# Performance work log

Measured on AMD Instinct MI355X. Metric: run time of the kernel, lower is better.

The kernel has to match this reference:

```python
import jax, jax.numpy as jnp
import numpy as np

B, S, D = 4, 1024, 1024      # batch, seq_len, hidden_size
I = 4096                     # intermediate_size
E = 8                        # num_experts
K = 2                        # top-k


def setup_inputs() -> dict:
    key = jax.random.key(0)
    ks = jax.random.split(key, 8)
    x = jax.random.normal(ks[0], (B, S, D), dtype=jnp.float32)
    gate_w = jax.random.normal(ks[1], (E, D), dtype=jnp.float32) * 0.02
    gate_b = jnp.zeros((E,), dtype=jnp.float32)
    w1 = jax.random.normal(ks[2], (E, I, D), dtype=jnp.float32) * 0.02
    b1 = jnp.zeros((E, I), dtype=jnp.float32)
    w2 = jax.random.normal(ks[3], (E, D, I), dtype=jnp.float32) * 0.02
    b2 = jnp.zeros((E, D), dtype=jnp.float32)
    return {"x": x, "gate_w": gate_w, "gate_b": gate_b,
            "w1": w1, "b1": b1, "w2": w2, "b2": b2}


def reference(x, gate_w, gate_b, w1, b1, w2, b2):
    b, s, d = x.shape
    xf = x.reshape(-1, d)                                  # [N, D]
    logits = xf @ gate_w.T + gate_b                        # [N, E]
    top_vals, top_idx = jax.lax.top_k(logits, K)           # [N, K]
    top_w = jax.nn.softmax(top_vals, axis=-1)              # softmax over the k selected logits

    # combine[n, e] = routing weight of token n for expert e (0 if not selected)
    n_tok = xf.shape[0]
    combine = jnp.zeros((n_tok, w1.shape[0]), dtype=x.dtype)
    combine = combine.at[jnp.arange(n_tok)[:, None], top_idx].add(top_w)

    out = jnp.zeros_like(xf)
    for e in range(w1.shape[0]):                           # small fixed loop over experts
        h = jax.nn.gelu(xf @ w1[e].T + b1[e], approximate=False)  # exact GELU (torch default)
        out = out + combine[:, e:e + 1] * (h @ w2[e].T + b2[e])
    return out.reshape(b, s, d)
```

## Files before the change

kernel.cpp:

```cpp
#include <hip/hip_runtime.h>
#include <math.h>

#define NTOK 4096
#define DDIM 1024
#define IDIM 4096
#define NEXP 8
#define MAXPAD 9216

typedef _Float16 f16x8 __attribute__((ext_vector_type(8)));
typedef _Float16 f16x4 __attribute__((ext_vector_type(4)));
typedef float    f32x4 __attribute__((ext_vector_type(4)));

__device__ __forceinline__ void glds16(const _Float16* g, _Float16* l) {
    __builtin_amdgcn_global_load_lds(
        (const __attribute__((address_space(1))) _Float16*)g,
        (__attribute__((address_space(3))) _Float16*)l, 16, 0, 0);
}

__device__ __forceinline__ float fast_gelu(float v) {
    float u = v * (0.7978845608f + 0.0356774081f * v * v);
    float ex = __builtin_amdgcn_exp2f(u * 2.8853900817779268f);
    float th = 1.0f - 2.0f * __builtin_amdgcn_rcpf(ex + 1.0f);
    return 0.5f * v * (1.0f + th);
}

__global__ void cvt_kernel(const float* __restrict__ src, _Float16* __restrict__ dst, int n4) {
    int i = blockIdx.x * blockDim.x + threadIdx.x;
    if (i >= n4) return;
    float4 v = ((const float4*)src)[i];
    f16x4 o = { (_Float16)v.x, (_Float16)v.y, (_Float16)v.z, (_Float16)v.w };
    ((f16x4*)dst)[i] = o;
}

__global__ void gate_kernel(const float* __restrict__ x, const float* __restrict__ gw,
                            const float* __restrict__ gb,
                            int* __restrict__ cnt, int* __restrict__ tok,
                            float* __restrict__ wgt) {
    int wave = threadIdx.x >> 6;
    int lane = threadIdx.x & 63;
    int token = blockIdx.x * 4 + wave;
    const float* xr = x + (size_t)token * DDIM;
    float xv[16];
#pragma unroll
    for (int j = 0; j < 16; ++j) xv[j] = xr[lane + 64 * j];
    float lg[NEXP];
#pragma unroll
    for (int e = 0; e < NEXP; ++e) {
        const float* g = gw + e * DDIM;
        float s = 0.f;
#pragma unroll
        for (int j = 0; j < 16; ++j) s += xv[j] * g[lane + 64 * j];
#pragma unroll
        for (int o = 32; o > 0; o >>= 1) s += __shfl_xor(s, o, 64);
        lg[e] = s + gb[e];
    }
    if (lane == 0) {
        int i0 = 0; float v0 = lg[0];
        for (int e = 1; e < NEXP; ++e) if (lg[e] > v0) { v0 = lg[e]; i0 = e; }
        int i1 = -1; float v1 = -3.0e38f;
        for (int e = 0; e < NEXP; ++e) { if (e == i0) continue; if (lg[e] > v1) { v1 = lg[e]; i1 = e; } }
        float e1 = expf(v1 - v0);
        float den = 1.f + e1;
        float w0 = 1.f / den;
        float w1 = e1 / den;
        int p0 = atomicAdd(&cnt[i0], 1);
        tok[i0 * NTOK + p0] = token; wgt[i0 * NTOK + p0] = w0;
        int p1 = atomicAdd(&cnt[i1], 1);
        tok[i1 * NTOK + p1] = token; wgt[i1 * NTOK + p1] = w1;
    }
}

__global__ void scan_kernel(const int* __restrict__ cnt, int* __restrict__ off) {
    if (threadIdx.x == 0) {
        int acc = 0;
        for (int e = 0; e < NEXP; ++e) { off[e] = acc; acc += ((cnt[e] + 127) >> 7) << 7; }
        off[NEXP] = acc;
    }
}

__global__ void gather_kernel(const float* __restrict__ x, const int* __restrict__ cnt,
                              const int* __restrict__ off, const int* __restrict__ tok,
                              _Float16* __restrict__ xg) {
    int row = blockIdx.x;
    if (row >= off[NEXP]) return;
    int e = 0;
    while (e < NEXP - 1 && row >= off[e + 1]) ++e;
    int r = row - off[e];
    int t = threadIdx.x;
    _Float16* dst = xg + (size_t)row * DDIM;
    if (r < cnt[e]) {
        int token = tok[e * NTOK + r];
        float4 v = ((const float4*)(x + (size_t)token * DDIM))[t];
        f16x4 o = { (_Float16)v.x, (_Float16)v.y, (_Float16)v.z, (_Float16)v.w };
        ((f16x4*)dst)[t] = o;
    } else {
        f16x4 z = {};
        ((f16x4*)dst)[t] = z;
    }
}

template <int KDIM, int NDIM, int NT, int EPI, int SPLIT>
__global__ __launch_bounds__(256, 4) void gemm_kernel(
    const _Float16* __restrict__ A,
    const _Float16* __restrict__ Bw,
    const float* __restrict__ bias,
    const int* __restrict__ cnt, const int* __restrict__ off,
    const int* __restrict__ tok, const float* __restrict__ wgt,
    _Float16* __restrict__ Hout, float* __restrict__ Out) {
    int e  = blockIdx.z / SPLIT;
    int kc = blockIdx.z % SPLIT;
    const int KB = KDIM / SPLIT;
    int nt = blockIdx.x % NT;
    int mt = blockIdx.x / NT;
    int ce = cnt[e];
    int mtiles = (ce + 127) >> 7;
    if (mt >= mtiles) return;
    int rowbase = off[e] + mt * 128;
    int colbase = nt * 128;

    __shared__ __align__(16) _Float16 As[128 * 32];
    __shared__ __align__(16) _Float16 Bs[128 * 32];

    int tid = threadIdx.x;
    int wv = tid >> 6, lane = tid & 63;
    int wm = (wv >> 1) * 64, wn = (wv & 1) * 64;

    const _Float16* Abase = A + (size_t)rowbase * KDIM + kc * KB;
    const _Float16* Bbase = Bw + (size_t)e * NDIM * KDIM + (size_t)colbase * KDIM + kc * KB;

    int ldrow = wv * 32 + (lane >> 2);
    int ldcol = (lane & 3) * 8;

    int fr = lane & 15;
    int fk = (lane >> 4) * 8;

    f32x4 acc[4][4] = {};

    for (int k0 = 0; k0 < KB; k0 += 32) {
        __syncthreads();
        glds16(Abase + (size_t)ldrow * KDIM + k0 + ldcol,        &As[(wv * 32) * 32]);
        glds16(Abase + (size_t)(ldrow + 16) * KDIM + k0 + ldcol, &As[(wv * 32 + 16) * 32]);
        glds16(Bbase + (size_t)ldrow * KDIM + k0 + ldcol,        &Bs[(wv * 32) * 32]);
        glds16(Bbase + (size_t)(ldrow + 16) * KDIM + k0 + ldcol, &Bs[(wv * 32 + 16) * 32]);
        __syncthreads();
        f16x8 a[4], b[4];
#pragma unroll
        for (int i = 0; i < 4; ++i) a[i] = *(const f16x8*)&As[(wm + i * 16 + fr) * 32 + fk];
#pragma unroll
        for (int j = 0; j < 4; ++j) b[j] = *(const f16x8*)&Bs[(wn + j * 16 + fr) * 32 + fk];
#pragma unroll
        for (int i = 0; i < 4; ++i)
#pragma unroll
            for (int j = 0; j < 4; ++j)
                acc[i][j] = __builtin_amdgcn_mfma_f32_16x16x32_f16(a[i], b[j], acc[i][j], 0, 0, 0);
    }

    int rquad = (lane >> 4) * 4;
    if (EPI == 1) {
#pragma unroll
        for (int i = 0; i < 4; ++i) {
#pragma unroll
            for (int j = 0; j < 4; ++j) {
                int col = colbase + wn + j * 16 + fr;
                float bb = bias[e * NDIM + col];
#pragma unroll
                for (int r = 0; r < 4; ++r) {
                    int ml = wm + i * 16 + rquad + r;
                    float v = fast_gelu(acc[i][j][r] + bb);
                    Hout[(size_t)(rowbase + ml) * NDIM + col] = (_Float16)v;
                }
            }
        }
    } else {
#pragma unroll
        for (int i = 0; i < 4; ++i) {
#pragma unroll
            for (int r = 0; r < 4; ++r) {
                int ml = wm + i * 16 + rquad + r;
                int slot = mt * 128 + ml;
                if (slot < ce) {
                    int token = tok[e * NTOK + slot];
                    float w = wgt[e * NTOK + slot];
#pragma unroll
                    for (int j = 0; j < 4; ++j) {
                        int col = colbase + wn + j * 16 + fr;
                        float v = acc[i][j][r];
                        if (kc == 0) v += bias[e * NDIM + col];
                        unsafeAtomicAdd(&Out[(size_t)token * NDIM + col], w * v);
                    }
                }
            }
        }
    }
}

extern "C" void kernel_launch(void* const* d_in, const int* in_sizes, int n_in,
                              void* d_out, int out_size, void* d_ws, size_t ws_size,
                              hipStream_t stream) {
    const float* x      = (const float*)d_in[0];
    const float* gate_w = (const float*)d_in[1];
    const float* gate_b = (const float*)d_in[2];
    const float* w1     = (const float*)d_in[3];
    const float* b1     = (const float*)d_in[4];
    const float* w2     = (const float*)d_in[5];
    const float* b2     = (const float*)d_in[6];
    float* out = (float*)d_out;

    char* p = (char*)d_ws;
    _Float16* w1h  = (_Float16*)p; p += (size_t)NEXP * IDIM * DDIM * 2;
    _Float16* w2h  = (_Float16*)p; p += (size_t)NEXP * DDIM * IDIM * 2;
    _Float16* xg   = (_Float16*)p; p += (size_t)MAXPAD * DDIM * 2;
    _Float16* hbuf = (_Float16*)p; p += (size_t)MAXPAD * IDIM * 2;
    int*      tok  = (int*)p;      p += (size_t)NEXP * NTOK * 4;
    float*    wgt  = (float*)p;    p += (size_t)NEXP * NTOK * 4;
    int*      cnt  = (int*)p;      p += 128;
    int*      off  = (int*)p;      p += 128;

    hipMemsetAsync(cnt, 0, 128, stream);
    hipMemsetAsync(out, 0, (size_t)NTOK * DDIM * 4, stream);

    cvt_kernel<<<32768, 256, 0, stream>>>(w1, w1h, NEXP * IDIM * DDIM / 4);
    cvt_kernel<<<32768, 256, 0, stream>>>(w2, w2h, NEXP * DDIM * IDIM / 4);
    gate_kernel<<<NTOK / 4, 256, 0, stream>>>(x, gate_w, gate_b, cnt, tok, wgt);
    scan_kernel<<<1, 64, 0, stream>>>(cnt, off);
    gather_kernel<<<MAXPAD, 256, 0, stream>>>(x, cnt, off, tok, xg);

    gemm_kernel<DDIM, IDIM, IDIM / 128, 1, 1><<<dim3(32 * (IDIM / 128), 1, NEXP), 256, 0, stream>>>(
        xg, w1h, b1, cnt, off, tok, wgt, hbuf, (float*)nullptr);
    gemm_kernel<IDIM, DDIM, DDIM / 128, 2, 4><<<dim3(32 * (DDIM / 128), 1, NEXP * 4), 256, 0, stream>>>(
        hbuf, w2h, b2, cnt, off, tok, wgt, (_Float16*)nullptr, out);
}
```

Before: 701.0 us.

## Use persistent GEMM blocks with atomic tile counter over real expert tiles

Precomputes per-expert tile offsets in the scan kernel and turns both expert GEMMs into persistent kernels with 1024 blocks that fetch work tiles from a global atomic counter. This removes the many empty blocks launched for worst-case padding and balances the uneven per-expert work. It adds an atomic and two barriers per tile, and tiles are taken in a fixed order that may reduce cache locality.

New measurement: 744.0 us. +6.1%, slower.

```diff
diff --git a/kernel.cpp b/kernel.cpp
--- a/kernel.cpp
+++ b/kernel.cpp
@@ -72,9 +72,14 @@
 
 __global__ void scan_kernel(const int* __restrict__ cnt, int* __restrict__ off) {
     if (threadIdx.x == 0) {
-        int acc = 0;
-        for (int e = 0; e < NEXP; ++e) { off[e] = acc; acc += ((cnt[e] + 127) >> 7) << 7; }
-        off[NEXP] = acc;
+        int acc = 0, t1 = 0, t2 = 0;
+        for (int e = 0; e < NEXP; ++e) {
+            int mtiles = (cnt[e] + 127) >> 7;
+            off[e] = acc;       acc += mtiles << 7;
+            off[10 + e] = t1;   t1 += mtiles * (IDIM / 128);
+            off[20 + e] = t2;   t2 += mtiles * (DDIM / 128) * 4;
+        }
+        off[NEXP] = acc; off[10 + NEXP] = t1; off[20 + NEXP] = t2;
     }
 }
 
@@ -106,87 +111,98 @@
     const float* __restrict__ bias,
     const int* __restrict__ cnt, const int* __restrict__ off,
     const int* __restrict__ tok, const float* __restrict__ wgt,
-    _Float16* __restrict__ Hout, float* __restrict__ Out) {
-    int e  = blockIdx.z / SPLIT;
-    int kc = blockIdx.z % SPLIT;
+    _Float16* __restrict__ Hout, float* __restrict__ Out,
+    int* __restrict__ counter, const int* __restrict__ toff) {
     const int KB = KDIM / SPLIT;
-    int nt = blockIdx.x % NT;
-    int mt = blockIdx.x / NT;
-    int ce = cnt[e];
-    int mtiles = (ce + 127) >> 7;
-    if (mt >= mtiles) return;
-    int rowbase = off[e] + mt * 128;
-    int colbase = nt * 128;
 
     __shared__ __align__(16) _Float16 As[128 * 32];
     __shared__ __align__(16) _Float16 Bs[128 * 32];
+    __shared__ int s_tile;
 
     int tid = threadIdx.x;
     int wv = tid >> 6, lane = tid & 63;
     int wm = (wv >> 1) * 64, wn = (wv & 1) * 64;
-
-    const _Float16* Abase = A + (size_t)rowbase * KDIM + kc * KB;
-    const _Float16* Bbase = Bw + (size_t)e * NDIM * KDIM + (size_t)colbase * KDIM + kc * KB;
-
     int ldrow = wv * 32 + (lane >> 2);
     int ldcol = (lane & 3) * 8;
-
     int fr = lane & 15;
     int fk = (lane >> 4) * 8;
-
-    f32x4 acc[4][4] = {};
-
-    for (int k0 = 0; k0 < KB; k0 += 32) {
+    int total = toff[NEXP];
+
+    while (true) {
         __syncthreads();
-        glds16(Abase + (size_t)ldrow * KDIM + k0 + ldcol,        &As[(wv * 32) * 32]);
-        glds16(Abase + (size_t)(ldrow + 16) * KDIM + k0 + ldcol, &As[(wv * 32 + 16) * 32]);
-        glds16(Bbase + (size_t)ldrow * KDIM + k0 + ldcol,        &Bs[(wv * 32) * 32]);
-        glds16(Bbase + (size_t)(ldrow + 16) * KDIM + k0 + ldcol, &Bs[(wv * 32 + 16) * 32]);
+        if (tid == 0) s_tile = atomicAdd(counter, 1);
         __syncthreads();
-        f16x8 a[4], b[4];
-#pragma unroll
-        for (int i = 0; i < 4; ++i) a[i] = *(const f16x8*)&As[(wm + i * 16 + fr) * 32 + fk];
-#pragma unroll
-        for (int j = 0; j < 4; ++j) b[j] = *(const f16x8*)&Bs[(wn + j * 16 + fr) * 32 + fk];
-#pragma unroll
-        for (int i = 0; i < 4; ++i)
-#pragma unroll
-            for (int j = 0; j < 4; ++j)
-                acc[i][j] = __builtin_amdgcn_mfma_f32_16x16x32_f16(a[i], b[j], acc[i][j], 0, 0, 0);
-    }
-
-    int rquad = (lane >> 4) * 4;
-    if (EPI == 1) {
-#pragma unroll
-        for (int i = 0; i < 4; ++i) {
-#pragma unroll
-            for (int j = 0; j < 4; ++j) {
-                int col = colbase + wn + j * 16 + fr;
-                float bb = bias[e * NDIM + col];
+        int t = s_tile;
+        if (t >= total) return;
+
+        int e = 0;
+        while (e < NEXP - 1 && t >= toff[e + 1]) ++e;
+        int local = t - toff[e];
+        int nt = local % NT;
+        int r2 = local / NT;
+        int kc = r2 % SPLIT;
+        int mt = r2 / SPLIT;
+
+        int ce = cnt[e];
+        int rowbase = off[e] + mt * 128;
+        int colbase = nt * 128;
+        const _Float16* Abase = A + (size_t)rowbase * KDIM + kc * KB;
+        const _Float16* Bbase = Bw + (size_t)e * NDIM * KDIM + (size_t)colbase * KDIM + kc * KB;
+
+        f32x4 acc[4][4] = {};
+
+        for (int k0 = 0; k0 < KB; k0 += 32) {
+            __syncthreads();
+            glds16(Abase + (size_t)ldrow * KDIM + k0 + ldcol,        &As[(wv * 32) * 32]);
+            glds16(Abase + (size_t)(ldrow + 16) * KDIM + k0 + ldcol, &As[(wv * 32 + 16) * 32]);
+            glds16(Bbase + (size_t)ldrow * KDIM + k0 + ldcol,        &Bs[(wv * 32) * 32]);
+            glds16(Bbase + (size_t)(ldrow + 16) * KDIM + k0 + ldcol, &Bs[(wv * 32 + 16) * 32]);
+            __syncthreads();
+            f16x8 a[4], b[4];
+#pragma unroll
+            for (int i = 0; i < 4; ++i) a[i] = *(const f16x8*)&As[(wm + i * 16 + fr) * 32 + fk];
+#pragma unroll
+            for (int j = 0; j < 4; ++j) b[j] = *(const f16x8*)&Bs[(wn + j * 16 + fr) * 32 + fk];
+#pragma unroll
+            for (int i = 0; i < 4; ++i)
+#pragma unroll
+                for (int j = 0; j < 4; ++j)
+                    acc[i][j] = __builtin_amdgcn_mfma_f32_16x16x32_f16(a[i], b[j], acc[i][j], 0, 0, 0);
+        }
+
+        int rquad = (lane >> 4) * 4;
+        if (EPI == 1) {
+#pragma unroll
+            for (int i = 0; i < 4; ++i) {
+#pragma unroll
+                for (int j = 0; j < 4; ++j) {
+                    int col = colbase + wn + j * 16 + fr;
+                    float bb = bias[e * NDIM + col];
+#pragma unroll
+                    for (int r = 0; r < 4; ++r) {
+                        int ml = wm + i * 16 + rquad + r;
+                        float v = fast_gelu(acc[i][j][r] + bb);
+                        Hout[(size_t)(rowbase + ml) * NDIM + col] = (_Float16)v;
+                    }
+                }
+            }
+        } else {
+#pragma unroll
+            for (int i = 0; i < 4; ++i) {
 #pragma unroll
                 for (int r = 0; r < 4; ++r) {
                     int ml = wm + i * 16 + rquad + r;
-                    float v = fast_gelu(acc[i][j][r] + bb);
-                    Hout[(size_t)(rowbase + ml) * NDIM + col] = (_Float16)v;
-                }
-            }
-        }
-    } else {
-#pragma unroll
-        for (int i = 0; i < 4; ++i) {
-#pragma unroll
-            for (int r = 0; r < 4; ++r) {
-                int ml = wm + i * 16 + rquad + r;
-                int slot = mt * 128 + ml;
-                if (slot < ce) {
-                    int token = tok[e * NTOK + slot];
-                    float w = wgt[e * NTOK + slot];
-#pragma unroll
-                    for (int j = 0; j < 4; ++j) {
-                        int col = colbase + wn + j * 16 + fr;
-                        float v = acc[i][j][r];
-                        if (kc == 0) v += bias[e * NDIM + col];
-                        unsafeAtomicAdd(&Out[(size_t)token * NDIM + col], w * v);
+                    int slot = mt * 128 + ml;
+                    if (slot < ce) {
+                        int token = tok[e * NTOK + slot];
+                        float w = wgt[e * NTOK + slot];
+#pragma unroll
+                        for (int j = 0; j < 4; ++j) {
+                            int col = colbase + wn + j * 16 + fr;
+                            float v = acc[i][j][r];
+                            if (kc == 0) v += bias[e * NDIM + col];
+                            unsafeAtomicAdd(&Out[(size_t)token * NDIM + col], w * v);
+                        }
                     }
                 }
             }
@@ -225,8 +241,8 @@
     scan_kernel<<<1, 64, 0, stream>>>(cnt, off);
     gather_kernel<<<MAXPAD, 256, 0, stream>>>(x, cnt, off, tok, xg);
 
-    gemm_kernel<DDIM, IDIM, IDIM / 128, 1, 1><<<dim3(32 * (IDIM / 128), 1, NEXP), 256, 0, stream>>>(
-        xg, w1h, b1, cnt, off, tok, wgt, hbuf, (float*)nullptr);
-    gemm_kernel<IDIM, DDIM, DDIM / 128, 2, 4><<<dim3(32 * (DDIM / 128), 1, NEXP * 4), 256, 0, stream>>>(
-        hbuf, w2h, b2, cnt, off, tok, wgt, (_Float16*)nullptr, out);
-}
+    gemm_kernel<DDIM, IDIM, IDIM / 128, 1, 1><<<1024, 256, 0, stream>>>(
+        xg, w1h, b1, cnt, off, tok, wgt, hbuf, (float*)nullptr, cnt + 8, off + 10);
+    gemm_kernel<IDIM, DDIM, DDIM / 128, 2, 4><<<1024, 256, 0, stream>>>(
+        hbuf, w2h, b2, cnt, off, tok, wgt, (_Float16*)nullptr, out, cnt + 12, off + 20);
+}
```
